# Performance work log

Measured on AMD Instinct MI355X. Metric: run time of the kernel, lower is better.

The kernel has to match this reference:

```python
import jax, jax.numpy as jnp
import numpy as np
import math

B, S, H, DM = 1, 2048, 16, 1024
DK = DM // H
MAX_SEQ = 2048  # rel_embed has MAX_SEQ+1 rows


def setup_inputs() -> dict:
    rng = jax.random.key(0)
    ks = jax.random.split(rng, 12)
    w = lambda k, shape, s=0.02: (jax.random.normal(k, shape, jnp.float32) * s)
    inp = {
        'query': jax.random.normal(ks[0], (B, S, DM), jnp.float32),
        'key':   jax.random.normal(ks[1], (B, S, DM), jnp.float32),
        'value': jax.random.normal(ks[2], (B, S, DM), jnp.float32),
        # causal integer mask [B,S,S] (cumsum over it derives rel-pos indices)
        'mask': jnp.broadcast_to(jnp.tril(jnp.ones((S, S), jnp.int32)), (B, S, S)),
        'Wq': w(ks[3], (DM, DM)), 'bq': jnp.zeros((DM,), jnp.float32),
        'Wk': w(ks[4], (DM, DM)), 'bk': jnp.zeros((DM,), jnp.float32),
        'Wv': w(ks[5], (DM, DM)), 'bv': jnp.zeros((DM,), jnp.float32),
        'Wo': w(ks[6], (DM, DM)), 'bo': jnp.zeros((DM,), jnp.float32),
        # relative position embeddings [h, max_seq_len+1, d_k], N(0,1) as in the module
        'rel_embed': jax.random.normal(ks[7], (H, MAX_SEQ + 1, DK), jnp.float32),
    }
    return inp


def reference(query, key, value, mask, Wq, bq, Wk, bk, Wv, bv, Wo, bo, rel_embed):
    scale = 1.0 / math.sqrt(DK)
    heads = lambda x, W, b: (x @ W.T + b).reshape(B, S, H, DK).transpose(0, 2, 1, 3)
    q = heads(query, Wq, bq)   # [B,H,S,DK]
    k = heads(key, Wk, bk)
    v = heads(value, Wv, bv)

    scores = jnp.einsum('bhid,bhjd->bhij', q, k) * scale  # [B,H,S,S]

    m4 = mask[:, None, :, :]                 # [B,1,S,S]
    nz = m4 != 0
    # torch: cumsum(mask)-1 picks the m-index; index 0 (then zeroed) where mask==0
    m_idx = jnp.where(nz, jnp.cumsum(m4, axis=-1) - 1, 0)  # [B,1,S,S]

    # rel_scores[b,h,m,l] = <q[b,h,l,:], rel_embed[h,m,:]> / sqrt(d_k)
    rel = jnp.einsum('bhld,hmd->bhml', q, rel_embed[:, :S]) * scale  # [B,H,S,S]
    idx = jnp.broadcast_to(m_idx, (B, H, S, S))
    # torch.take flat-index decodes to rel[b,h, m_idx[i,j], j]
    rel_g = jnp.take_along_axis(rel, idx, axis=2) * nz.astype(scores.dtype)

    scores = jnp.where(nz, scores + rel_g, jnp.float32(-1e9))
    p = jax.nn.softmax(scores, axis=-1)      # dropout p=0.0 -> identity

    out = jnp.einsum('bhij,bhjd->bhid', p, v)         # [B,H,S,DK]
    out = out.transpose(0, 2, 1, 3).reshape(B, S, DM)  # [B,S,DM]
    return out @ Wo.T + bo
```

## Files before the change

### kernel.cpp

```cpp
#include <hip/hip_runtime.h>

typedef __bf16 bf16_t;
typedef __bf16 bf16x4 __attribute__((ext_vector_type(4)));
typedef __bf16 bf16x8 __attribute__((ext_vector_type(8)));
typedef float  f32x4  __attribute__((ext_vector_type(4)));
typedef float  f32x16 __attribute__((ext_vector_type(16)));
typedef unsigned int u32;

#define S_LEN 2048
#define DMODEL 1024
#define NHEAD 16
#define DHEAD 64
#define RELROWS 2049

__device__ __forceinline__ void gload16(const void* g, void* l) {
    __builtin_amdgcn_global_load_lds((const __attribute__((address_space(1))) void*)g,
                                     (__attribute__((address_space(3))) void*)l,
                                     16, 0, 0);
}

__device__ __forceinline__ f32x4 mfma16(bf16x8 a, bf16x8 b, f32x4 c) {
    return __builtin_amdgcn_mfma_f32_16x16x32_bf16(a, b, c, 0, 0, 0);
}
__device__ __forceinline__ f32x16 mfma32(bf16x8 a, bf16x8 b, f32x16 c) {
    return __builtin_amdgcn_mfma_f32_32x32x16_bf16(a, b, c, 0, 0, 0);
}

__device__ __forceinline__ bf16x8 lds_read_swz(const bf16_t* base, int row, int colb) {
    return *(const bf16x8*)((const char*)base + row * 128 + (colb ^ ((row & 7) << 4)));
}
__device__ __forceinline__ bf16x8 lds_read_swz32(const bf16_t* base, int row, int colb) {
    return *(const bf16x8*)((const char*)base + row * 64 + (colb ^ (((row >> 1) & 3) << 4)));
}

__device__ __forceinline__ u32 cvtpk(float lo, float hi) {
    u32 w;
    asm("v_cvt_pk_bf16_f32 %0, %1, %2" : "=v"(w) : "v"(lo), "v"(hi));
    return w;
}
__device__ __forceinline__ void swap32(u32& a, u32& b) {
    asm("v_permlane32_swap_b32 %0, %1" : "+v"(a), "+v"(b));
}
__device__ __forceinline__ float fexp2(float x) {
    float r;
    asm("v_exp_f32 %0, %1" : "=v"(r) : "v"(x));
    return r;
}

__global__ __launch_bounds__(256)
void f2bf_all(const float* __restrict__ xq, const float* __restrict__ xk,
              const float* __restrict__ xv,
              const float* __restrict__ wq, const float* __restrict__ wk,
              const float* __restrict__ wv, const float* __restrict__ wo,
              bf16_t* __restrict__ dst, int n4X, int n4W) {
    const int i = blockIdx.x * blockDim.x + threadIdx.x;
    const float* src; int j;
    if (i < 3 * n4X) {
        if (i < n4X)            { src = xq; j = i; }
        else if (i < 2 * n4X)   { src = xk; j = i - n4X; }
        else                    { src = xv; j = i - 2 * n4X; }
    } else {
        int w = i - 3 * n4X;
        if (w < n4W)            { src = wq; j = w; }
        else if (w < 2 * n4W)   { src = wk; j = w - n4W; }
        else if (w < 3 * n4W)   { src = wv; j = w - 2 * n4W; }
        else                    { src = wo; j = w - 3 * n4W; }
    }
    float4 v = ((const float4*)src)[j];
    bf16x4 o;
    o[0] = (bf16_t)v.x; o[1] = (bf16_t)v.y; o[2] = (bf16_t)v.z; o[3] = (bf16_t)v.w;
    ((bf16x4*)dst)[i] = o;
}

template <int BM, int BN>
__global__ __launch_bounds__(256)
void gemm_qkv(const bf16_t* __restrict__ Abase, const bf16_t* __restrict__ Wbase,
              const float* __restrict__ b0, const float* __restrict__ b1,
              const float* __restrict__ b2,
              bf16_t* __restrict__ outb,
              const float* __restrict__ relp, float* __restrict__ RGout,
              bf16_t* __restrict__ vtp,
              int M, int N, int K) {
    __shared__ alignas(16) bf16_t As[4][BM * 32];
    __shared__ alignas(16) bf16_t Bs[4][BN * 32];
    const int tid = threadIdx.x, lane = tid & 63, wave = tid >> 6;
    const int z = blockIdx.z;
    const bf16_t* A = Abase + (size_t)z * M * K;
    const bf16_t* W = Wbase + (size_t)z * N * K;
    const float* bias = (z == 0) ? b0 : (z == 1 ? b1 : b2);
    const int nwg = gridDim.x * gridDim.y;
    const int wg = blockIdx.y * gridDim.x + blockIdx.x;
    const int swz = (wg & 7) * (nwg >> 3) + (wg >> 3);
    const int m0 = (swz / gridDim.x) * BM, n0 = (swz % gridDim.x) * BN;
    const int wr = (wave >> 1) * (BM / 2), wc = (wave & 1) * (BN / 2);
    constexpr int MR = BM / 32, NR = BN / 32;

    f32x4 acc[MR][NR] = {};

    auto stage = [&](int b, int kt) {
#pragma unroll
        for (int r = 0; r < 2; ++r) {
            int rr = wave * 2 + r;
            int L = rr * 1024 + lane * 16;
            int row = L >> 6;
            int colb = (L & 63) ^ (((row >> 1) & 3) << 4);
            gload16(A + (size_t)(m0 + row) * K + kt + (colb >> 1),
                    (char*)As[b] + rr * 1024);
        }
        {
            int rr = wave;
            int L = rr * 1024 + lane * 16;
            int row = L >> 6;
            int colb = (L & 63) ^ (((row >> 1) & 3) << 4);
            gload16(W + (size_t)(n0 + row) * K + kt + (colb >> 1),
                    (char*)Bs[b] + rr * 1024);
        }
    };

    const int NH = K >> 5;
    stage(0, 0); stage(1, 32); stage(2, 64);
    for (int s = 0; s < NH; ++s) {
        if (s + 2 < NH)      asm volatile("s_waitcnt vmcnt(6)" ::: "memory");
        else if (s + 1 < NH) asm volatile("s_waitcnt vmcnt(3)" ::: "memory");
        else                 asm volatile("s_waitcnt vmcnt(0)" ::: "memory");
        asm volatile("s_barrier" ::: "memory");
        if (s + 3 < NH) stage((s + 3) & 3, (s + 3) << 5);
        const int buf = s & 3;
        bf16x8 af[MR], bfr[NR];
#pragma unroll
        for (int m = 0; m < MR; ++m)
            af[m] = lds_read_swz32(As[buf], wr + m * 16 + (lane & 15), (lane >> 4) * 16);
#pragma unroll
        for (int n = 0; n < NR; ++n)
            bfr[n] = lds_read_swz32(Bs[buf], wc + n * 16 + (lane & 15), (lane >> 4) * 16);
        __builtin_amdgcn_s_setprio(1);
#pragma unroll
        for (int m = 0; m < MR; ++m)
#pragma unroll
            for (int n = 0; n < NR; ++n)
                acc[m][n] = mfma16(af[m], bfr[n], acc[m][n]);
        __builtin_amdgcn_s_setprio(0);
    }

    const float scale = (z == 0) ? 0.18033688011112042f : 1.0f;
    float rp[MR][4];
#pragma unroll
    for (int m = 0; m < MR; ++m)
#pragma unroll
        for (int r2 = 0; r2 < 4; ++r2) rp[m][r2] = 0.f;
    const int hh = n0 >> 6;
#pragma unroll
    for (int m = 0; m < MR; ++m) {
        const int gi = m0 + wr + m * 16 + (lane >> 4) * 4;
#pragma unroll
        for (int n = 0; n < NR; ++n) {
            const int gj = n0 + wc + n * 16 + (lane & 15);
            const float bv = bias[gj];
            if (z == 2) {
                bf16x4 o4;
#pragma unroll
                for (int r2 = 0; r2 < 4; ++r2) o4[r2] = (bf16_t)(acc[m][n][r2] + bv);
                *(bf16x4*)&vtp[(size_t)gj * S_LEN + gi] = o4;
            } else {
#pragma unroll
                for (int r2 = 0; r2 < 4; ++r2) {
                    float v = (acc[m][n][r2] + bv) * scale;
                    outb[(size_t)z * M * N + (size_t)(gi + r2) * N + gj] = (bf16_t)v;
                    if (z == 0)
                        rp[m][r2] += v * relp[((size_t)hh * RELROWS + (gi + r2)) * DHEAD + (gj & 63)];
                }
            }
        }
    }
    if (z == 0) {
        constexpr int HM = BM / 2;
        float* Rp = (float*)As;
#pragma unroll
        for (int m = 0; m < MR; ++m)
#pragma unroll
            for (int r2 = 0; r2 < 4; ++r2) {
                float p = rp[m][r2];
                p += __shfl_xor(p, 1);
                p += __shfl_xor(p, 2);
                p += __shfl_xor(p, 4);
                p += __shfl_xor(p, 8);
                if ((lane & 15) == 0)
                    Rp[wave * HM + m * 16 + (lane >> 4) * 4 + r2] = p;
            }
        __syncthreads();
        if ((wave & 1) == 0) {
#pragma unroll
            for (int rr0 = 0; rr0 < HM; rr0 += 64) {
                int rr = rr0 + lane;
                float v = Rp[wave * HM + rr] + Rp[(wave + 1) * HM + rr];
                RGout[hh * S_LEN + m0 + wr + rr] = v;
            }
        }
    }
}

__global__ __launch_bounds__(512)
void gemm_out(const bf16_t* __restrict__ A, const bf16_t* __restrict__ W,
              const float* __restrict__ bias, float* __restrict__ outf,
              int M, int N, int K) {
    __shared__ alignas(16) bf16_t As[2][2][64 * 64];
    __shared__ alignas(16) bf16_t Bs[2][2][64 * 64];
    const int tid = threadIdx.x, lane = tid & 63, wave = tid >> 6;
    const int grp = wave >> 2, w4 = wave & 3;
    const int nwg = gridDim.x * gridDim.y;
    const int wg = blockIdx.y * gridDim.x + blockIdx.x;
    const int swz = (wg & 7) * (nwg >> 3) + (wg >> 3);
    const int m0 = (swz / gridDim.x) * 64, n0 = (swz % gridDim.x) * 64;
    const int wr = (w4 >> 1) * 32, wc = (w4 & 1) * 32;
    const int kbase = grp * (K >> 1);

    f32x4 acc[2][2] = {};
    const int soff = w4 * 1024 + lane * 16;

    auto stage = [&](int b, int kt) {
#pragma unroll
        for (int r = 0; r < 2; ++r) {
            int L = r * 4096 + soff;
            int row = L >> 7, colb = (L & 127) ^ ((row & 7) << 4);
            gload16(A + (size_t)(m0 + row) * K + kt + (colb >> 1),
                    (char*)As[grp][b] + r * 4096 + w4 * 1024);
            gload16(W + (size_t)(n0 + row) * K + kt + (colb >> 1),
                    (char*)Bs[grp][b] + r * 4096 + w4 * 1024);
        }
    };

    const int NKg = K >> 7;
    stage(0, kbase);
    for (int s = 0; s < NKg; ++s) {
        const int buf = s & 1;
        if (s + 1 < NKg) {
            stage(buf ^ 1, kbase + ((s + 1) << 6));
            asm volatile("s_waitcnt vmcnt(4)" ::: "memory");
        } else {
            asm volatile("s_waitcnt vmcnt(0)" ::: "memory");
        }
        asm volatile("s_barrier" ::: "memory");
#pragma unroll
        for (int kk = 0; kk < 2; ++kk) {
            bf16x8 af[2], bfr[2];
#pragma unroll
            for (int m = 0; m < 2; ++m)
                af[m] = lds_read_swz(As[grp][buf], wr + m * 16 + (lane & 15),
                                     kk * 64 + (lane >> 4) * 16);
#pragma unroll
            for (int n = 0; n < 2; ++n)
                bfr[n] = lds_read_swz(Bs[grp][buf], wc + n * 16 + (lane & 15),
                                      kk * 64 + (lane >> 4) * 16);
#pragma unroll
            for (int m = 0; m < 2; ++m)
#pragma unroll
                for (int n = 0; n < 2; ++n)
                    acc[m][n] = mfma16(af[m], bfr[n], acc[m][n]);
        }
        asm volatile("s_barrier" ::: "memory");
    }

    float* scr = (float*)As;
    if (grp == 1) {
        float* base = scr + ((w4 * 64 + lane) << 4);
#pragma unroll
        for (int m = 0; m < 2; ++m)
#pragma unroll
            for (int n = 0; n < 2; ++n)
                *(f32x4*)(base + (m * 2 + n) * 4) = acc[m][n];
    }
    __syncthreads();
    if (grp == 0) {
        const float* base = scr + ((w4 * 64 + lane) << 4);
#pragma unroll
        for (int m = 0; m < 2; ++m) {
            const int gi = m0 + wr + m * 16 + (lane >> 4) * 4;
#pragma unroll
            for (int n = 0; n < 2; ++n) {
                f32x4 ov = *(const f32x4*)(base + (m * 2 + n) * 4);
                const int gj = n0 + wc + n * 16 + (lane & 15);
                const float bv = bias[gj];
#pragma unroll
                for (int r2 = 0; r2 < 4; ++r2)
                    outf[(size_t)(gi + r2) * N + gj] = acc[m][n][r2] + ov[r2] + bv;
            }
        }
    }
}

__global__ __launch_bounds__(256, 2)
void flash_attn(const bf16_t* __restrict__ Qb, const bf16_t* __restrict__ Kb,
                const bf16_t* __restrict__ Vtp, const float* __restrict__ RG,
                bf16_t* __restrict__ Ob) {
    __shared__ alignas(16) bf16_t KB[4][64 * 64];
    __shared__ alignas(16) bf16_t VB[4][64 * 64];
    __shared__ alignas(16) float Rs[S_LEN];
    const int tid = threadIdx.x, lane = tid & 63, wave = tid >> 6;
    const int h = blockIdx.x;
    const int qt = (int)gridDim.y - 1 - (int)blockIdx.y;
    const int q0 = qt * 32;
    const int nt = (qt >> 1) + 1;
    const int qpar = qt & 1;
    const int lo5 = lane & 31, hi = lane >> 5;

    const int nkv = nt * 64;
    for (int i = tid * 8; i < nkv; i += 2048) {
        *(float4*)&Rs[i]     = *(const float4*)&RG[h * S_LEN + i];
        *(float4*)&Rs[i + 4] = *(const float4*)&RG[h * S_LEN + i + 4];
    }

    const bf16_t* qp = Qb + (size_t)(q0 + lo5) * DMODEL + h * DHEAD;
    bf16x8 qf[4];
#pragma unroll
    for (int c = 0; c < 4; ++c)
        qf[c] = *(const bf16x8*)(qp + c * 16 + hi * 8);

    auto stageK = [&](int tt) {
        char* dst = (char*)KB[wave];
#pragma unroll
        for (int rr = 0; rr < 8; ++rr) {
            int L = rr * 1024 + lane * 16;
            int row = L >> 7, colb = (L & 127) ^ ((row & 7) << 4);
            gload16(Kb + (size_t)(tt * 64 + row) * DMODEL + h * DHEAD + (colb >> 1),
                    dst + rr * 1024);
        }
    };
    auto stageV = [&](int tt) {
        char* dst = (char*)VB[wave];
#pragma unroll
        for (int rr = 0; rr < 8; ++rr) {
            int L = rr * 1024 + lane * 16;
            int row = L >> 7, colb = (L & 127) ^ ((row & 7) << 4);
            gload16(Vtp + (size_t)(h * DHEAD + row) * S_LEN + tt * 64 + (colb >> 1),
                    dst + rr * 1024);
        }
    };

    if (wave < nt) { stageK(wave); stageV(wave); }
    __syncthreads();

    f32x16 oacc[2] = {};
    float ls = 0.f;
    const int thr = qpar * 32 + lo5;

    for (int tt = wave; tt < nt; tt += 4) {
        const int kv0 = tt * 64;
        const bool diag = (tt == nt - 1);
        asm volatile("s_waitcnt vmcnt(8)" ::: "memory");

        f32x16 sta, stb;
#pragma unroll
        for (int g = 0; g < 4; ++g) {
            f32x4 ra = *(const f32x4*)&Rs[kv0 + g * 8 + hi * 4];
            f32x4 rb = *(const f32x4*)&Rs[kv0 + 32 + g * 8 + hi * 4];
#pragma unroll
            for (int e = 0; e < 4; ++e) { sta[g * 4 + e] = ra[e]; stb[g * 4 + e] = rb[e]; }
        }
        __builtin_amdgcn_s_setprio(1);
#pragma unroll
        for (int c = 0; c < 4; ++c) {
            bf16x8 kfa = lds_read_swz(KB[wave], lo5, c * 32 + hi * 16);
            sta = mfma32(kfa, qf[c], sta);
        }
#pragma unroll
        for (int c = 0; c < 4; ++c) {
            bf16x8 kfb = lds_read_swz(KB[wave], 32 + lo5, c * 32 + hi * 16);
            stb = mfma32(kfb, qf[c], stb);
        }
        __builtin_amdgcn_s_setprio(0);
        if (tt + 4 < nt) stageK(tt + 4);

        float pra[16], prb[16];
        if (diag) {
#pragma unroll
            for (int r = 0; r < 16; ++r) {
                int kloc = (r & 3) + 8 * (r >> 2) + 4 * hi;
                float va = fexp2(sta[r]), vb = fexp2(stb[r]);
                pra[r] = (kloc > thr) ? 0.f : va;
                prb[r] = (kloc + 32 > thr) ? 0.f : vb;
            }
        } else {
#pragma unroll
            for (int r = 0; r < 16; ++r) { pra[r] = fexp2(sta[r]); prb[r] = fexp2(stb[r]); }
        }
#pragma unroll
        for (int r = 0; r < 16; ++r) ls += pra[r] + prb[r];
        u32 pw[4][4];
#pragma unroll
        for (int hf = 0; hf < 2; ++hf) {
            u32 a  = cvtpk(pra[8 * hf + 0], pra[8 * hf + 1]);
            u32 b  = cvtpk(pra[8 * hf + 4], pra[8 * hf + 5]);
            swap32(a, b);
            u32 c2 = cvtpk(pra[8 * hf + 2], pra[8 * hf + 3]);
            u32 d2 = cvtpk(pra[8 * hf + 6], pra[8 * hf + 7]);
            swap32(c2, d2);
            pw[hf][0] = a;  pw[hf][1] = c2;  pw[hf][2] = b;  pw[hf][3] = d2;
        }
#pragma unroll
        for (int hf = 0; hf < 2; ++hf) {
            u32 a  = cvtpk(prb[8 * hf + 0], prb[8 * hf + 1]);
            u32 b  = cvtpk(prb[8 * hf + 4], prb[8 * hf + 5]);
            swap32(a, b);
            u32 c2 = cvtpk(prb[8 * hf + 2], prb[8 * hf + 3]);
            u32 d2 = cvtpk(prb[8 * hf + 6], prb[8 * hf + 7]);
            swap32(c2, d2);
            pw[2 + hf][0] = a;  pw[2 + hf][1] = c2;  pw[2 + hf][2] = b;  pw[2 + hf][3] = d2;
        }

        if (tt + 4 < nt) asm volatile("s_waitcnt vmcnt(8)" ::: "memory");
        else             asm volatile("s_waitcnt vmcnt(0)" ::: "memory");

        __builtin_amdgcn_s_setprio(1);
#pragma unroll
        for (int kc = 0; kc < 4; ++kc) {
            union { u32 w[4]; bf16x8 v; } uu;
            uu.w[0] = pw[kc][0]; uu.w[1] = pw[kc][1]; uu.w[2] = pw[kc][2]; uu.w[3] = pw[kc][3];
#pragma unroll
            for (int db = 0; db < 2; ++db) {
                bf16x8 vf = lds_read_swz(VB[wave], db * 32 + lo5, kc * 32 + hi * 16);
                oacc[db] = mfma32(vf, uu.v, oacc[db]);
            }
        }
        __builtin_amdgcn_s_setprio(0);
        if (tt + 4 < nt) stageV(tt + 4);
    }

    asm volatile("s_waitcnt vmcnt(0)" ::: "memory");
    __syncthreads();
    float* scr = (float*)KB;
    if (wave > 0) {
        float* base = scr + (wave - 1) * 2112 + lane * 32;
#pragma unroll
        for (int db = 0; db < 2; ++db)
#pragma unroll
            for (int g = 0; g < 4; ++g) {
                f32x4 v4;
#pragma unroll
                for (int e = 0; e < 4; ++e) v4[e] = oacc[db][g * 4 + e];
                *(f32x4*)(base + db * 16 + g * 4) = v4;
            }
        scr[(wave - 1) * 2112 + 2048 + lane] = ls;
    }
    __syncthreads();
    if (wave == 0) {
#pragma unroll
        for (int w2 = 0; w2 < 3; ++w2) {
            const float* base = scr + w2 * 2112 + lane * 32;
#pragma unroll
            for (int db = 0; db < 2; ++db)
#pragma unroll
                for (int g = 0; g < 4; ++g) {
                    f32x4 v4 = *(const f32x4*)(base + db * 16 + g * 4);
#pragma unroll
                    for (int e = 0; e < 4; ++e) oacc[db][g * 4 + e] += v4[e];
                }
            ls += scr[w2 * 2112 + 2048 + lane];
        }
        ls += __shfl_xor(ls, 32);
        const float inv = 1.0f / ls;
        const int qg = q0 + lo5;
#pragma unroll
        for (int db = 0; db < 2; ++db)
#pragma unroll
            for (int g = 0; g < 4; ++g) {
                bf16x4 o4;
#pragma unroll
                for (int e = 0; e < 4; ++e)
                    o4[e] = (bf16_t)(oacc[db][g * 4 + e] * inv);
                *(bf16x4*)&Ob[(size_t)qg * DMODEL + h * DHEAD + db * 32 + g * 8 + hi * 4] = o4;
            }
    }
}

extern "C" void kernel_launch(void* const* d_in, const int* in_sizes, int n_in,
                              void* d_out, int out_size, void* d_ws, size_t ws_size,
                              hipStream_t stream) {
    const float* query = (const float*)d_in[0];
    const float* key   = (const float*)d_in[1];
    const float* value = (const float*)d_in[2];
    const float* Wq  = (const float*)d_in[4];
    const float* bq  = (const float*)d_in[5];
    const float* Wk  = (const float*)d_in[6];
    const float* bk  = (const float*)d_in[7];
    const float* Wv  = (const float*)d_in[8];
    const float* bv  = (const float*)d_in[9];
    const float* Wo  = (const float*)d_in[10];
    const float* bo  = (const float*)d_in[11];
    const float* rel = (const float*)d_in[12];

    char* ws = (char*)d_ws;
    const size_t nX = (size_t)S_LEN * DMODEL;
    const size_t nW = (size_t)DMODEL * DMODEL;
    bf16_t* Xbf  = (bf16_t*)ws;
    bf16_t* Wbf  = (bf16_t*)(ws + 3 * nX * 2);
    bf16_t* QKV  = (bf16_t*)(ws + 3 * nX * 2 + 4 * nW * 2);
    float*  RG   = (float*)(ws + 3 * nX * 2 + 4 * nW * 2 + 3 * nX * 2);
    bf16_t* Vtp  = QKV + 2 * nX;
    bf16_t* AOb  = (bf16_t*)(ws + nX * 2);
    (void)in_sizes; (void)n_in; (void)out_size; (void)ws_size;

    const int n4X = (int)(nX / 4), n4W = (int)(nW / 4);
    const int tot4 = 3 * n4X + 4 * n4W;
    f2bf_all<<<tot4 / 256, 256, 0, stream>>>(query, key, value, Wq, Wk, Wv, Wo,
                                             Xbf, n4X, n4W);

    gemm_qkv<128, 64><<<dim3(DMODEL / 64, S_LEN / 128, 3), 256, 0, stream>>>(
        Xbf, Wbf, bq, bk, bv, QKV, rel, RG, Vtp, S_LEN, DMODEL, DMODEL);

    flash_attn<<<dim3(NHEAD, S_LEN / 32), 256, 0, stream>>>(QKV, QKV + nX, Vtp, RG, AOb);

    gemm_out<<<dim3(DMODEL / 64, S_LEN / 64), 512, 0, stream>>>(
        AOb, Wbf + 3 * nW, bo, (float*)d_out, S_LEN, DMODEL, DMODEL);
}
```

Measured before the change: 85.46 us.

## Split QKV GEMM K-dimension across waves with LDS reduction; grid-stride conversion kernel

The QKV projection GEMM now uses 64x64 tiles, doubling the block count. Each of the four waves computes the full tile over its own quarter of K, using private double-buffered LDS staging with no block barriers in the main loop. The partial accumulators are then reduced through LDS by wave 0, which runs the bias, scale, rel-pos and store epilogue alone. This trades barrier sync and occupancy limits for an LDS reduction step and a single-wave epilogue. The fp32-to-bf16 conversion kernel also switches to a fixed 2048-block grid-stride loop.

```diff
diff --git a/kernel.cpp b/kernel.cpp
--- a/kernel.cpp
+++ b/kernel.cpp
@@ -52,28 +52,29 @@
               const float* __restrict__ xv,
               const float* __restrict__ wq, const float* __restrict__ wk,
               const float* __restrict__ wv, const float* __restrict__ wo,
-              bf16_t* __restrict__ dst, int n4X, int n4W) {
-    const int i = blockIdx.x * blockDim.x + threadIdx.x;
-    const float* src; int j;
-    if (i < 3 * n4X) {
-        if (i < n4X)            { src = xq; j = i; }
-        else if (i < 2 * n4X)   { src = xk; j = i - n4X; }
-        else                    { src = xv; j = i - 2 * n4X; }
-    } else {
-        int w = i - 3 * n4X;
-        if (w < n4W)            { src = wq; j = w; }
-        else if (w < 2 * n4W)   { src = wk; j = w - n4W; }
-        else if (w < 3 * n4W)   { src = wv; j = w - 2 * n4W; }
-        else                    { src = wo; j = w - 3 * n4W; }
-    }
-    float4 v = ((const float4*)src)[j];
-    bf16x4 o;
-    o[0] = (bf16_t)v.x; o[1] = (bf16_t)v.y; o[2] = (bf16_t)v.z; o[3] = (bf16_t)v.w;
-    ((bf16x4*)dst)[i] = o;
-}
-
-template <int BM, int BN>
-__global__ __launch_bounds__(256)
+              bf16_t* __restrict__ dst, int n4X, int n4W, int tot4) {
+    for (int i = blockIdx.x * blockDim.x + threadIdx.x; i < tot4;
+         i += gridDim.x * blockDim.x) {
+        const float* src; int j;
+        if (i < 3 * n4X) {
+            if (i < n4X)            { src = xq; j = i; }
+            else if (i < 2 * n4X)   { src = xk; j = i - n4X; }
+            else                    { src = xv; j = i - 2 * n4X; }
+        } else {
+            int w = i - 3 * n4X;
+            if (w < n4W)            { src = wq; j = w; }
+            else if (w < 2 * n4W)   { src = wk; j = w - n4W; }
+            else if (w < 3 * n4W)   { src = wv; j = w - 2 * n4W; }
+            else                    { src = wo; j = w - 3 * n4W; }
+        }
+        float4 v = ((const float4*)src)[j];
+        bf16x4 o;
+        o[0] = (bf16_t)v.x; o[1] = (bf16_t)v.y; o[2] = (bf16_t)v.z; o[3] = (bf16_t)v.w;
+        ((bf16x4*)dst)[i] = o;
+    }
+}
+
+__global__ __launch_bounds__(256, 2)
 void gemm_qkv(const bf16_t* __restrict__ Abase, const bf16_t* __restrict__ Wbase,
               const float* __restrict__ b0, const float* __restrict__ b1,
               const float* __restrict__ b2,
@@ -81,8 +82,7 @@
               const float* __restrict__ relp, float* __restrict__ RGout,
               bf16_t* __restrict__ vtp,
               int M, int N, int K) {
-    __shared__ alignas(16) bf16_t As[4][BM * 32];
-    __shared__ alignas(16) bf16_t Bs[4][BN * 32];
+    __shared__ alignas(16) bf16_t PB[4][8192];
     const int tid = threadIdx.x, lane = tid & 63, wave = tid >> 6;
     const int z = blockIdx.z;
     const bf16_t* A = Abase + (size_t)z * M * K;
@@ -91,70 +91,98 @@
     const int nwg = gridDim.x * gridDim.y;
     const int wg = blockIdx.y * gridDim.x + blockIdx.x;
     const int swz = (wg & 7) * (nwg >> 3) + (wg >> 3);
-    const int m0 = (swz / gridDim.x) * BM, n0 = (swz % gridDim.x) * BN;
-    const int wr = (wave >> 1) * (BM / 2), wc = (wave & 1) * (BN / 2);
-    constexpr int MR = BM / 32, NR = BN / 32;
-
-    f32x4 acc[MR][NR] = {};
-
-    auto stage = [&](int b, int kt) {
-#pragma unroll
-        for (int r = 0; r < 2; ++r) {
-            int rr = wave * 2 + r;
+    const int m0 = (swz / gridDim.x) * 64, n0 = (swz % gridDim.x) * 64;
+    const int kq = wave * (K >> 2);
+    char* reg = (char*)PB[wave];
+
+    auto stageA = [&](int b, int kt) {
+#pragma unroll
+        for (int rr = 0; rr < 4; ++rr) {
             int L = rr * 1024 + lane * 16;
             int row = L >> 6;
             int colb = (L & 63) ^ (((row >> 1) & 3) << 4);
             gload16(A + (size_t)(m0 + row) * K + kt + (colb >> 1),
-                    (char*)As[b] + rr * 1024);
-        }
-        {
-            int rr = wave;
+                    reg + b * 4096 + rr * 1024);
+        }
+    };
+    auto stageB = [&](int b, int kt) {
+#pragma unroll
+        for (int rr = 0; rr < 4; ++rr) {
             int L = rr * 1024 + lane * 16;
             int row = L >> 6;
             int colb = (L & 63) ^ (((row >> 1) & 3) << 4);
             gload16(W + (size_t)(n0 + row) * K + kt + (colb >> 1),
-                    (char*)Bs[b] + rr * 1024);
+                    reg + 8192 + b * 4096 + rr * 1024);
         }
     };
 
-    const int NH = K >> 5;
-    stage(0, 0); stage(1, 32); stage(2, 64);
-    for (int s = 0; s < NH; ++s) {
-        if (s + 2 < NH)      asm volatile("s_waitcnt vmcnt(6)" ::: "memory");
-        else if (s + 1 < NH) asm volatile("s_waitcnt vmcnt(3)" ::: "memory");
-        else                 asm volatile("s_waitcnt vmcnt(0)" ::: "memory");
-        asm volatile("s_barrier" ::: "memory");
-        if (s + 3 < NH) stage((s + 3) & 3, (s + 3) << 5);
-        const int buf = s & 3;
-        bf16x8 af[MR], bfr[NR];
-#pragma unroll
-        for (int m = 0; m < MR; ++m)
-            af[m] = lds_read_swz32(As[buf], wr + m * 16 + (lane & 15), (lane >> 4) * 16);
-#pragma unroll
-        for (int n = 0; n < NR; ++n)
-            bfr[n] = lds_read_swz32(Bs[buf], wc + n * 16 + (lane & 15), (lane >> 4) * 16);
+    f32x4 acc[4][4] = {};
+    const int NS = K >> 7;
+    stageA(0, kq); stageB(0, kq);
+    for (int s = 0; s < NS; ++s) {
+        const int buf = s & 1;
+        if (s + 1 < NS) {
+            stageA(buf ^ 1, kq + (s + 1) * 32);
+            stageB(buf ^ 1, kq + (s + 1) * 32);
+            asm volatile("s_waitcnt vmcnt(8)" ::: "memory");
+        } else {
+            asm volatile("s_waitcnt vmcnt(0)" ::: "memory");
+        }
+        const bf16_t* Abuf = (const bf16_t*)(reg + buf * 4096);
+        const bf16_t* Bbuf = (const bf16_t*)(reg + 8192 + buf * 4096);
+        bf16x8 af[4], bfr[4];
+#pragma unroll
+        for (int m = 0; m < 4; ++m)
+            af[m] = lds_read_swz32(Abuf, m * 16 + (lane & 15), (lane >> 4) * 16);
+#pragma unroll
+        for (int n = 0; n < 4; ++n)
+            bfr[n] = lds_read_swz32(Bbuf, n * 16 + (lane & 15), (lane >> 4) * 16);
         __builtin_amdgcn_s_setprio(1);
 #pragma unroll
-        for (int m = 0; m < MR; ++m)
-#pragma unroll
-            for (int n = 0; n < NR; ++n)
+        for (int m = 0; m < 4; ++m)
+#pragma unroll
+            for (int n = 0; n < 4; ++n)
                 acc[m][n] = mfma16(af[m], bfr[n], acc[m][n]);
         __builtin_amdgcn_s_setprio(0);
     }
 
+    if (wave > 0) {
+        char* base = reg;
+#pragma unroll
+        for (int m = 0; m < 4; ++m)
+#pragma unroll
+            for (int n = 0; n < 4; ++n)
+                *(f32x4*)(base + (m * 4 + n) * 1024 + lane * 16) = acc[m][n];
+    }
+    __syncthreads();
+    if (wave != 0) return;
+
+#pragma unroll
+    for (int w2 = 1; w2 < 4; ++w2) {
+        const char* base = (const char*)PB[w2];
+#pragma unroll
+        for (int m = 0; m < 4; ++m)
+#pragma unroll
+            for (int n = 0; n < 4; ++n) {
+                f32x4 v4 = *(const f32x4*)(base + (m * 4 + n) * 1024 + lane * 16);
+#pragma unroll
+                for (int e = 0; e < 4; ++e) acc[m][n][e] += v4[e];
+            }
+    }
+
     const float scale = (z == 0) ? 0.18033688011112042f : 1.0f;
-    float rp[MR][4];
-#pragma unroll
-    for (int m = 0; m < MR; ++m)
+    const int hh = n0 >> 6;
+    float rp[4][4];
+#pragma unroll
+    for (int m = 0; m < 4; ++m)
 #pragma unroll
         for (int r2 = 0; r2 < 4; ++r2) rp[m][r2] = 0.f;
-    const int hh = n0 >> 6;
-#pragma unroll
-    for (int m = 0; m < MR; ++m) {
-        const int gi = m0 + wr + m * 16 + (lane >> 4) * 4;
-#pragma unroll
-        for (int n = 0; n < NR; ++n) {
-            const int gj = n0 + wc + n * 16 + (lane & 15);
+#pragma unroll
+    for (int m = 0; m < 4; ++m) {
+        const int gi = m0 + m * 16 + (lane >> 4) * 4;
+#pragma unroll
+        for (int n = 0; n < 4; ++n) {
+            const int gj = n0 + n * 16 + (lane & 15);
             const float bv = bias[gj];
             if (z == 2) {
                 bf16x4 o4;
@@ -173,10 +201,8 @@
         }
     }
     if (z == 0) {
-        constexpr int HM = BM / 2;
-        float* Rp = (float*)As;
-#pragma unroll
-        for (int m = 0; m < MR; ++m)
+#pragma unroll
+        for (int m = 0; m < 4; ++m)
 #pragma unroll
             for (int r2 = 0; r2 < 4; ++r2) {
                 float p = rp[m][r2];
@@ -185,17 +211,8 @@
                 p += __shfl_xor(p, 4);
                 p += __shfl_xor(p, 8);
                 if ((lane & 15) == 0)
-                    Rp[wave * HM + m * 16 + (lane >> 4) * 4 + r2] = p;
-            }
-        __syncthreads();
-        if ((wave & 1) == 0) {
-#pragma unroll
-            for (int rr0 = 0; rr0 < HM; rr0 += 64) {
-                int rr = rr0 + lane;
-                float v = Rp[wave * HM + rr] + Rp[(wave + 1) * HM + rr];
-                RGout[hh * S_LEN + m0 + wr + rr] = v;
-            }
-        }
+                    RGout[hh * S_LEN + m0 + m * 16 + (lane >> 4) * 4 + r2] = p;
+            }
     }
 }
 
@@ -501,10 +518,10 @@
 
     const int n4X = (int)(nX / 4), n4W = (int)(nW / 4);
     const int tot4 = 3 * n4X + 4 * n4W;
-    f2bf_all<<<tot4 / 256, 256, 0, stream>>>(query, key, value, Wq, Wk, Wv, Wo,
-                                             Xbf, n4X, n4W);
-
-    gemm_qkv<128, 64><<<dim3(DMODEL / 64, S_LEN / 128, 3), 256, 0, stream>>>(
+    f2bf_all<<<2048, 256, 0, stream>>>(query, key, value, Wq, Wk, Wv, Wo,
+                                       Xbf, n4X, n4W, tot4);
+
+    gemm_qkv<<<dim3(DMODEL / 64, S_LEN / 64, 3), 256, 0, stream>>>(
         Xbf, Wbf, bq, bk, bv, QKV, rel, RG, Vtp, S_LEN, DMODEL, DMODEL);
 
     flash_attn<<<dim3(NHEAD, S_LEN / 32), 256, 0, stream>>>(QKV, QKV + nX, Vtp, RG, AOb);
```

Result: slower. 104.1 us (+21.8%).
